# Performance work log

Hardware: AMD Instinct MI355X
Metric: run time of the kernel (lower is better)

## Reference

```python
import jax, jax.numpy as jnp
import numpy as np

D = 2048
H = 16
HD = D // H


def setup_inputs() -> dict:
    key = jax.random.key(0)
    k1, k2, k3 = jax.random.split(key, 3)
    x = jax.random.normal(k1, (2, 2048, D), dtype=jnp.float32)
    # torch Linear(d, 3d, bias=False): y = x @ W.T; store transposed weight [D, 3D]
    Wqkv = jax.random.normal(k2, (D, 3 * D), dtype=jnp.float32) * (D ** -0.5)
    Wo = jax.random.normal(k3, (D, D), dtype=jnp.float32) * (D ** -0.5)
    return {"x": x, "Wqkv": Wqkv, "Wo": Wo}


def reference(x, Wqkv, Wo):
    B, S, _ = x.shape
    qkv = (x @ Wqkv).reshape(B, S, 3, H, HD)
    q = qkv[:, :, 0].transpose(0, 2, 1, 3)  # [B,H,S,HD]
    k = qkv[:, :, 1].transpose(0, 2, 1, 3)
    v = qkv[:, :, 2].transpose(0, 2, 1, 3)
    scores = jnp.einsum("bhqd,bhkd->bhqk", q, k) * (HD ** -0.5)
    causal = jnp.tril(jnp.ones((S, S), dtype=bool))  # keep lower triangle
    scores = jnp.where(causal, scores, jnp.float32(-1e9))
    a = jax.nn.softmax(scores, axis=-1)
    o = jnp.einsum("bhqk,bhkd->bhqd", a, v)
    o = o.transpose(0, 2, 1, 3).reshape(B, S, H * HD)
    return o @ Wo
```

## Files before the change

kernel.cpp:

```cpp
#include <hip/hip_runtime.h>
#include <hip/hip_bf16.h>
#include <cstdint>

typedef __bf16 bf16;
typedef __bf16 bf16x8 __attribute__((ext_vector_type(8)));
typedef __bf16 bf16x4 __attribute__((ext_vector_type(4)));
typedef __bf16 bf16x2 __attribute__((ext_vector_type(2)));
typedef float floatx4 __attribute__((ext_vector_type(4)));
typedef float f32x16 __attribute__((ext_vector_type(16)));
typedef int intx4 __attribute__((ext_vector_type(4)));

#define MFMA16(a, b, c) __builtin_amdgcn_mfma_f32_16x16x32_bf16(a, b, c, 0, 0, 0)
#define MFMA32(a, b, c) __builtin_amdgcn_mfma_f32_32x32x16_bf16(a, b, c, 0, 0, 0)

__device__ __forceinline__ void gload_lds16(const void* g, void* l) {
    __builtin_amdgcn_global_load_lds(
        (const __attribute__((address_space(1))) void*)g,
        (__attribute__((address_space(3))) void*)l, 16, 0, 0);
}

__device__ __forceinline__ int pack2(float a, float b) {
    union { bf16x2 v; int u; } z;
    z.v[0] = (bf16)a;
    z.v[1] = (bf16)b;
    return z.u;
}

__global__ void downcast_kernel(const float* __restrict__ in, bf16* __restrict__ out,
                                size_t n) {
    const size_t i = ((size_t)blockIdx.x * blockDim.x + threadIdx.x) * 4;
    if (i >= n) return;
    const float4 v = *(const float4*)(in + i);
    bf16x4 o = {(bf16)v.x, (bf16)v.y, (bf16)v.z, (bf16)v.w};
    *(bf16x4*)(out + i) = o;
}

__global__ void transpose_kernel(const float* __restrict__ in, bf16* __restrict__ out,
                                 int R, int C) {
    __shared__ float tile[32][33];
    const int c0 = blockIdx.x * 32, r0 = blockIdx.y * 32;
    const int tx = threadIdx.x & 31, ty = threadIdx.x >> 5;
    for (int i = 0; i < 32; i += 8)
        tile[ty + i][tx] = in[(size_t)(r0 + ty + i) * C + (c0 + tx)];
    __syncthreads();
    for (int i = 0; i < 32; i += 8)
        out[(size_t)(c0 + ty + i) * R + (r0 + tx)] = (bf16)tile[tx][ty + i];
}

template <int MODE>
__global__ __launch_bounds__(256) void gemm_bt_kernel(
    const bf16* __restrict__ A, const bf16* __restrict__ BT,
    int M, int N, int K,
    bf16* __restrict__ qt, bf16* __restrict__ kt, bf16* __restrict__ vt,
    float* __restrict__ Cout) {
    __shared__ alignas(16) bf16 As[128 * 64];
    __shared__ alignas(16) bf16 Bs[128 * 64];

    const int tid = threadIdx.x;
    const int wave = tid >> 6, lane = tid & 63;
    const int quad = lane >> 4, r16 = lane & 15;
    const int m0 = blockIdx.y * 128, n0 = blockIdx.x * 128;
    const int wm = (wave >> 1) * 64, wn = (wave & 1) * 64;

    int srow[4], soff[4];
#pragma unroll
    for (int j = 0; j < 4; ++j) {
        const int c = tid + j * 256;
        srow[j] = c >> 3;
        soff[j] = ((c & 7) ^ (srow[j] & 7)) * 8;
    }

    floatx4 acc[4][4] = {};

    for (int k0 = 0; k0 < K; k0 += 64) {
        __syncthreads();
#pragma unroll
        for (int j = 0; j < 4; ++j) {
            const int c = tid + j * 256;
            gload_lds16(A + (size_t)(m0 + srow[j]) * K + k0 + soff[j], As + c * 8);
            gload_lds16(BT + (size_t)(n0 + srow[j]) * K + k0 + soff[j], Bs + c * 8);
        }
        __syncthreads();

#pragma unroll
        for (int kc = 0; kc < 2; ++kc) {
            bf16x8 a[4], b[4];
#pragma unroll
            for (int i = 0; i < 4; ++i) {
                const int row = wm + i * 16 + r16;
                const int sp = (4 * kc + quad) ^ (row & 7);
                a[i] = *(const bf16x8*)(As + row * 64 + sp * 8);
            }
#pragma unroll
            for (int j = 0; j < 4; ++j) {
                const int row = wn + j * 16 + r16;
                const int sp = (4 * kc + quad) ^ (row & 7);
                b[j] = *(const bf16x8*)(Bs + row * 64 + sp * 8);
            }
#pragma unroll
            for (int i = 0; i < 4; ++i)
#pragma unroll
                for (int j = 0; j < 4; ++j)
                    acc[i][j] = MFMA16(a[i], b[j], acc[i][j]);
        }
    }

    if (MODE == 0) {
        const int t = n0 >> 11;
        const float qscale = 0.08838834764831845f;
#pragma unroll
        for (int i = 0; i < 4; ++i) {
            const int mbase = m0 + wm + i * 16 + quad * 4;
            const int b_ = mbase >> 11;
            const int s = mbase & 2047;
#pragma unroll
            for (int j = 0; j < 4; ++j) {
                const int n = n0 + wn + j * 16 + r16;
                const int h = (n >> 7) & 15, hd = n & 127;
                const int bh = b_ * 16 + h;
                if (t == 0) {
#pragma unroll
                    for (int r = 0; r < 4; ++r)
                        qt[(size_t)(bh * 2048 + s + r) * 128 + hd] =
                            (bf16)(acc[i][j][r] * qscale);
                } else if (t == 1) {
#pragma unroll
                    for (int r = 0; r < 4; ++r)
                        kt[(size_t)(bh * 2048 + s + r) * 128 + hd] = (bf16)acc[i][j][r];
                } else {
                    bf16x4 pv = {(bf16)acc[i][j][0], (bf16)acc[i][j][1],
                                 (bf16)acc[i][j][2], (bf16)acc[i][j][3]};
                    *(bf16x4*)(vt + (size_t)(bh * 128 + hd) * 2048 + s) = pv;
                }
            }
        }
    } else {
#pragma unroll
        for (int i = 0; i < 4; ++i) {
            const int mbase = m0 + wm + i * 16 + quad * 4;
#pragma unroll
            for (int j = 0; j < 4; ++j) {
                const int n = n0 + wn + j * 16 + r16;
#pragma unroll
                for (int r = 0; r < 4; ++r)
                    Cout[(size_t)(mbase + r) * N + n] = acc[i][j][r];
            }
        }
    }
}

__global__ __launch_bounds__(256, 2) void attn_kernel(
    const bf16* __restrict__ qt, const bf16* __restrict__ kt,
    const bf16* __restrict__ vt, bf16* __restrict__ o) {
    __shared__ alignas(16) bf16 Ks[2][64 * 128];
    __shared__ alignas(16) bf16 Vts[2][128 * 64];

    const int tid = threadIdx.x;
    const int wave = tid >> 6, lane = tid & 63;
    const int l31 = lane & 31, h = lane >> 5;
    const int bh = blockIdx.x, by = blockIdx.y;
    const int t = by < 8 ? by : 23 - by;
    const int b_ = bh >> 4, hh = bh & 15;

    const int q0 = t * 128;
    const int qbase = q0 + wave * 32;
    const int qrow = qbase + l31;

    bf16x8 aq[8];
    {
        const bf16* qr = qt + (((size_t)bh * 2048 + qrow) << 7);
#pragma unroll
        for (int s = 0; s < 8; ++s)
            aq[s] = *(const bf16x8*)(qr + s * 16 + h * 8);
    }

    auto stageKV = [&](int buf, int k0) {
#pragma unroll
        for (int j = 0; j < 4; ++j) {
            const int c = tid + j * 256;
            const int row = c >> 4, sp = c & 15, s = sp ^ (row & 15);
            gload_lds16(kt + (((size_t)bh * 2048 + k0 + row) << 7) + s * 8,
                        &Ks[buf][c * 8]);
        }
#pragma unroll
        for (int j = 0; j < 4; ++j) {
            const int c = tid + j * 256;
            const int row = c >> 3, sp = c & 7, s = sp ^ (row & 7);
            gload_lds16(vt + ((size_t)bh * 128 + row) * 2048 + k0 + s * 8,
                        &Vts[buf][c * 8]);
        }
    };

    f32x16 oacc[4] = {};
    float lsum = 0.f;

    const int nit = 2 * t + 2;
    stageKV(0, 0);
    __syncthreads();
    int cur = 0;

    for (int it = 0; it < nit; ++it) {
        if (it + 1 < nit) stageKV(cur ^ 1, (it + 1) * 64);
        const int k0 = it * 64;

        if (k0 <= qbase + 31) {
            const bf16* Kc = &Ks[cur][0];
            const bf16* Vc = &Vts[cur][0];

            f32x16 sacc[2] = {};
            __builtin_amdgcn_s_setprio(1);
#pragma unroll
            for (int nt = 0; nt < 2; ++nt) {
#pragma unroll
                for (int s = 0; s < 8; ++s) {
                    const int sp = (2 * s + h) ^ (l31 & 15);
                    bf16x8 bk = *(const bf16x8*)(Kc + (nt * 32 + l31) * 128 + sp * 8);
                    sacc[nt] = MFMA32(bk, aq[s], sacc[nt]);
                }
            }
            __builtin_amdgcn_s_setprio(0);

            const bool needmask = (k0 + 63) > qbase;
            bf16x8 ap[4];
#pragma unroll
            for (int s4 = 0; s4 < 4; ++s4) {
                const int nt = s4 >> 1, base = (s4 & 1) * 8;
                float e[8];
#pragma unroll
                for (int k = 0; k < 8; ++k) {
                    const int c = base + k;
                    const int key = k0 + nt * 32 + (c & 3) + 8 * (c >> 2) + 4 * h;
                    float v = __expf(sacc[nt][c]);
                    if (needmask && key > qrow) v = 0.f;
                    e[k] = v;
                    lsum += v;
                }
                const int X0 = pack2(e[0], e[1]), X1 = pack2(e[2], e[3]);
                const int Y0 = pack2(e[4], e[5]), Y1 = pack2(e[6], e[7]);
                int W0 = h ? X0 : Y0, W1 = h ? X1 : Y1;
                W0 = __shfl_xor(W0, 32);
                W1 = __shfl_xor(W1, 32);
                union { intx4 w; bf16x8 v; } u;
                u.w[0] = h ? W0 : X0;
                u.w[1] = h ? W1 : X1;
                u.w[2] = h ? Y0 : W0;
                u.w[3] = h ? Y1 : W1;
                ap[s4] = u.v;
            }

            __builtin_amdgcn_s_setprio(1);
#pragma unroll
            for (int d0 = 0; d0 < 4; ++d0) {
#pragma unroll
                for (int ks = 0; ks < 4; ++ks) {
                    const int sp = (2 * ks + h) ^ (l31 & 7);
                    bf16x8 bv = *(const bf16x8*)(Vc + (d0 * 32 + l31) * 64 + sp * 8);
                    oacc[d0] = MFMA32(ap[ks], bv, oacc[d0]);
                }
            }
            __builtin_amdgcn_s_setprio(0);
        }

        __syncthreads();
        cur ^= 1;
    }

    lsum += __shfl_xor(lsum, 32);
    const float inv = 1.0f / lsum;
    float invr[16];
#pragma unroll
    for (int r = 0; r < 16; ++r)
        invr[r] = __shfl(inv, (r & 3) + 8 * (r >> 2) + 4 * h, 32);

#pragma unroll
    for (int d0 = 0; d0 < 4; ++d0) {
#pragma unroll
        for (int r = 0; r < 16; ++r) {
            const int rr = (r & 3) + 8 * (r >> 2) + 4 * h;
            o[(size_t)(b_ * 2048 + qbase + rr) * 2048 + hh * 128 + d0 * 32 + l31] =
                (bf16)(oacc[d0][r] * invr[r]);
        }
    }
}

extern "C" void kernel_launch(void* const* d_in, const int* in_sizes, int n_in,
                              void* d_out, int out_size, void* d_ws, size_t ws_size,
                              hipStream_t stream) {
    const float* x    = (const float*)d_in[0];
    const float* Wqkv = (const float*)d_in[1];
    const float* Wo   = (const float*)d_in[2];
    float* out        = (float*)d_out;

    char* ws = (char*)d_ws;
    bf16* xb    = (bf16*)ws; ws += (size_t)4096 * 2048 * 2;
    bf16* WqkvT = (bf16*)ws; ws += (size_t)6144 * 2048 * 2;
    bf16* WoT   = (bf16*)ws; ws += (size_t)2048 * 2048 * 2;
    bf16* qt    = (bf16*)ws; ws += (size_t)32 * 2048 * 128 * 2;
    bf16* kt    = (bf16*)ws; ws += (size_t)32 * 2048 * 128 * 2;
    bf16* vt    = (bf16*)ws; ws += (size_t)32 * 128 * 2048 * 2;
    bf16* ob    = (bf16*)ws; ws += (size_t)4096 * 2048 * 2;

    downcast_kernel<<<8192, 256, 0, stream>>>(x, xb, (size_t)4096 * 2048);
    transpose_kernel<<<dim3(192, 64), 256, 0, stream>>>(Wqkv, WqkvT, 2048, 6144);
    transpose_kernel<<<dim3(64, 64), 256, 0, stream>>>(Wo, WoT, 2048, 2048);

    gemm_bt_kernel<0><<<dim3(48, 32), 256, 0, stream>>>(
        xb, WqkvT, 4096, 6144, 2048, qt, kt, vt, nullptr);

    attn_kernel<<<dim3(32, 16), 256, 0, stream>>>(qt, kt, vt, ob);

    gemm_bt_kernel<1><<<dim3(16, 32), 256, 0, stream>>>(
        ob, WoT, 4096, 2048, 2048, nullptr, nullptr, nullptr, out);
}
```

Baseline: 375.2 us.

## Add 256x256 double-buffered QKV GEMM and fuse prep kernels into one launch

Replaces the 128x128 QKV projection GEMM with a 512-thread 256x256 tile kernel. It double-buffers LDS via direct global-to-LDS loads, uses XOR swizzling, raises priority around MFMA phases, and remaps blocks in a swizzled order for L2 locality. The downcast and two transpose kernels are merged into one launch to cut launch overhead. The larger tile raises arithmetic intensity, at the cost of 128KB LDS and one block per CU with only 384 blocks. The epilogue also applies the query scale at store time.

Measured after the change: 387.4 us. +3.3%, slower.

```diff
diff --git a/kernel.cpp b/kernel.cpp
--- a/kernel.cpp
+++ b/kernel.cpp
@@ -19,6 +19,11 @@
         (__attribute__((address_space(3))) void*)l, 16, 0, 0);
 }
 
+#define BARRIER()     asm volatile("s_barrier" ::: "memory")
+#define WAIT_LGKM0()  do { asm volatile("s_waitcnt lgkmcnt(0)" ::: "memory"); \
+                           __builtin_amdgcn_sched_barrier(0); } while (0)
+#define WAIT_VM(N)    asm volatile("s_waitcnt vmcnt(" #N ")" ::: "memory")
+
 __device__ __forceinline__ int pack2(float a, float b) {
     union { bf16x2 v; int u; } z;
     z.v[0] = (bf16)a;
@@ -26,25 +31,207 @@
     return z.u;
 }
 
-__global__ void downcast_kernel(const float* __restrict__ in, bf16* __restrict__ out,
-                                size_t n) {
-    const size_t i = ((size_t)blockIdx.x * blockDim.x + threadIdx.x) * 4;
-    if (i >= n) return;
-    const float4 v = *(const float4*)(in + i);
-    bf16x4 o = {(bf16)v.x, (bf16)v.y, (bf16)v.z, (bf16)v.w};
-    *(bf16x4*)(out + i) = o;
-}
-
-__global__ void transpose_kernel(const float* __restrict__ in, bf16* __restrict__ out,
-                                 int R, int C) {
+__global__ __launch_bounds__(256) void prep_kernel(
+    const float* __restrict__ x, const float* __restrict__ Wqkv,
+    const float* __restrict__ Wo, bf16* __restrict__ xb,
+    bf16* __restrict__ WqkvT, bf16* __restrict__ WoT) {
     __shared__ float tile[32][33];
-    const int c0 = blockIdx.x * 32, r0 = blockIdx.y * 32;
-    const int tx = threadIdx.x & 31, ty = threadIdx.x >> 5;
+    const int bid = blockIdx.x;
+    const int tid = threadIdx.x;
+
+    if (bid < 8192) {
+        const size_t i = ((size_t)bid * 256 + tid) * 4;
+        const float4 v = *(const float4*)(x + i);
+        bf16x4 o = {(bf16)v.x, (bf16)v.y, (bf16)v.z, (bf16)v.w};
+        *(bf16x4*)(xb + i) = o;
+        return;
+    }
+
+    const float* in;
+    bf16* out;
+    int R, C, bx, by;
+    if (bid < 20480) {
+        const int b = bid - 8192;
+        in = Wqkv; out = WqkvT; R = 2048; C = 6144;
+        bx = b % 192; by = b / 192;
+    } else {
+        const int b = bid - 20480;
+        in = Wo; out = WoT; R = 2048; C = 2048;
+        bx = b & 63; by = b >> 6;
+    }
+    const int c0 = bx * 32, r0 = by * 32;
+    const int tx = tid & 31, ty = tid >> 5;
     for (int i = 0; i < 32; i += 8)
         tile[ty + i][tx] = in[(size_t)(r0 + ty + i) * C + (c0 + tx)];
     __syncthreads();
     for (int i = 0; i < 32; i += 8)
         out[(size_t)(c0 + ty + i) * R + (r0 + tx)] = (bf16)tile[tx][ty + i];
+}
+
+__global__ __launch_bounds__(512, 1) void gemm256_qkv_kernel(
+    const bf16* __restrict__ A, const bf16* __restrict__ BT, int K,
+    bf16* __restrict__ qt, bf16* __restrict__ kt, bf16* __restrict__ vt) {
+    __shared__ alignas(16) bf16 As[2][16384];
+    __shared__ alignas(16) bf16 Bs[2][16384];
+
+    const int tid = threadIdx.x;
+    const int wave = tid >> 6, lane = tid & 63;
+    const int quad = lane >> 4, r16 = lane & 15;
+
+    const int flat = blockIdx.y * 24 + blockIdx.x;
+    const int swz = (flat & 7) * 48 + (flat >> 3);
+    const int n0 = (swz % 24) << 8, m0 = (swz / 24) << 8;
+
+    const int wm = (wave >> 2) << 7;
+    const int wn = (wave & 3) << 6;
+
+    auto stageTile = [&](int buf, int kt_) {
+#pragma unroll
+        for (int hf = 0; hf < 2; ++hf)
+#pragma unroll
+            for (int j = 0; j < 2; ++j) {
+                const int c = tid + j * 512;
+                const int row = c >> 3;
+                const int soff = ((c & 7) ^ (row & 7)) * 8;
+                gload_lds16(A + (size_t)(m0 + hf * 128 + row) * K + kt_ * 64 + soff,
+                            &As[buf][hf * 8192 + c * 8]);
+            }
+#pragma unroll
+        for (int hf = 0; hf < 2; ++hf)
+#pragma unroll
+            for (int j = 0; j < 2; ++j) {
+                const int c = tid + j * 512;
+                const int row = c >> 3;
+                const int soff = ((c & 7) ^ (row & 7)) * 8;
+                gload_lds16(BT + (size_t)(n0 + hf * 128 + row) * K + kt_ * 64 + soff,
+                            &Bs[buf][hf * 8192 + c * 8]);
+            }
+    };
+
+    floatx4 acc[8][4] = {};
+    const int NT = K >> 6;
+
+    stageTile(0, 0);
+    stageTile(1, 1);
+    WAIT_VM(8);
+    BARRIER();
+
+    for (int t = 0; t < NT; ++t) {
+        const int bsel = t & 1;
+        const bf16* Ab = &As[bsel][0];
+        const bf16* Bb = &Bs[bsel][0];
+        bf16x8 alo[4][2], ahi[4][2], blo[2][2], bhi[2][2];
+
+#pragma unroll
+        for (int i = 0; i < 4; ++i) {
+            const int row = wm + i * 16 + r16;
+#pragma unroll
+            for (int kc = 0; kc < 2; ++kc)
+                alo[i][kc] = *(const bf16x8*)(Ab + row * 64 + (((4 * kc + quad) ^ (row & 7)) << 3));
+        }
+#pragma unroll
+        for (int j = 0; j < 2; ++j) {
+            const int row = wn + j * 16 + r16;
+#pragma unroll
+            for (int kc = 0; kc < 2; ++kc)
+                blo[j][kc] = *(const bf16x8*)(Bb + row * 64 + (((4 * kc + quad) ^ (row & 7)) << 3));
+        }
+        BARRIER();
+        WAIT_LGKM0();
+        __builtin_amdgcn_s_setprio(1);
+#pragma unroll
+        for (int i = 0; i < 4; ++i)
+#pragma unroll
+            for (int j = 0; j < 2; ++j)
+#pragma unroll
+                for (int kc = 0; kc < 2; ++kc)
+                    acc[i][j] = MFMA16(alo[i][kc], blo[j][kc], acc[i][j]);
+        __builtin_amdgcn_s_setprio(0);
+        BARRIER();
+
+#pragma unroll
+        for (int j = 0; j < 2; ++j) {
+            const int row = wn + (2 + j) * 16 + r16;
+#pragma unroll
+            for (int kc = 0; kc < 2; ++kc)
+                bhi[j][kc] = *(const bf16x8*)(Bb + row * 64 + (((4 * kc + quad) ^ (row & 7)) << 3));
+        }
+        BARRIER();
+        WAIT_LGKM0();
+        __builtin_amdgcn_s_setprio(1);
+#pragma unroll
+        for (int i = 0; i < 4; ++i)
+#pragma unroll
+            for (int j = 0; j < 2; ++j)
+#pragma unroll
+                for (int kc = 0; kc < 2; ++kc)
+                    acc[i][2 + j] = MFMA16(alo[i][kc], bhi[j][kc], acc[i][2 + j]);
+        __builtin_amdgcn_s_setprio(0);
+        BARRIER();
+
+#pragma unroll
+        for (int i = 0; i < 4; ++i) {
+            const int row = wm + (4 + i) * 16 + r16;
+#pragma unroll
+            for (int kc = 0; kc < 2; ++kc)
+                ahi[i][kc] = *(const bf16x8*)(Ab + row * 64 + (((4 * kc + quad) ^ (row & 7)) << 3));
+        }
+        BARRIER();
+        WAIT_LGKM0();
+        __builtin_amdgcn_s_setprio(1);
+#pragma unroll
+        for (int i = 0; i < 4; ++i)
+#pragma unroll
+            for (int j = 0; j < 2; ++j)
+#pragma unroll
+                for (int kc = 0; kc < 2; ++kc)
+                    acc[4 + i][2 + j] = MFMA16(ahi[i][kc], bhi[j][kc], acc[4 + i][2 + j]);
+        __builtin_amdgcn_s_setprio(0);
+        BARRIER();
+
+        if (t + 2 < NT) stageTile(bsel, t + 2);
+        __builtin_amdgcn_s_setprio(1);
+#pragma unroll
+        for (int i = 0; i < 4; ++i)
+#pragma unroll
+            for (int j = 0; j < 2; ++j)
+#pragma unroll
+                for (int kc = 0; kc < 2; ++kc)
+                    acc[4 + i][j] = MFMA16(ahi[i][kc], blo[j][kc], acc[4 + i][j]);
+        __builtin_amdgcn_s_setprio(0);
+        if (t + 2 < NT) WAIT_VM(8);
+        else           WAIT_VM(0);
+        BARRIER();
+    }
+
+    const int tsel = n0 >> 11;
+    const float qscale = 0.08838834764831845f;
+#pragma unroll
+    for (int i = 0; i < 8; ++i) {
+        const int mbase = m0 + wm + i * 16 + quad * 4;
+        const int b_ = mbase >> 11;
+        const int s = mbase & 2047;
+#pragma unroll
+        for (int j = 0; j < 4; ++j) {
+            const int n = n0 + wn + j * 16 + r16;
+            const int h = (n >> 7) & 15, hd = n & 127;
+            const int bh = b_ * 16 + h;
+            if (tsel == 0) {
+#pragma unroll
+                for (int r = 0; r < 4; ++r)
+                    qt[(size_t)(bh * 2048 + s + r) * 128 + hd] =
+                        (bf16)(acc[i][j][r] * qscale);
+            } else if (tsel == 1) {
+#pragma unroll
+                for (int r = 0; r < 4; ++r)
+                    kt[(size_t)(bh * 2048 + s + r) * 128 + hd] = (bf16)acc[i][j][r];
+            } else {
+                bf16x4 pv = {(bf16)acc[i][j][0], (bf16)acc[i][j][1],
+                             (bf16)acc[i][j][2], (bf16)acc[i][j][3]};
+                *(bf16x4*)(vt + (size_t)(bh * 128 + hd) * 2048 + s) = pv;
+            }
+        }
+    }
 }
 
 template <int MODE>
@@ -300,12 +487,10 @@
     bf16* vt    = (bf16*)ws; ws += (size_t)32 * 128 * 2048 * 2;
     bf16* ob    = (bf16*)ws; ws += (size_t)4096 * 2048 * 2;
 
-    downcast_kernel<<<8192, 256, 0, stream>>>(x, xb, (size_t)4096 * 2048);
-    transpose_kernel<<<dim3(192, 64), 256, 0, stream>>>(Wqkv, WqkvT, 2048, 6144);
-    transpose_kernel<<<dim3(64, 64), 256, 0, stream>>>(Wo, WoT, 2048, 2048);
-
-    gemm_bt_kernel<0><<<dim3(48, 32), 256, 0, stream>>>(
-        xb, WqkvT, 4096, 6144, 2048, qt, kt, vt, nullptr);
+    prep_kernel<<<24576, 256, 0, stream>>>(x, Wqkv, Wo, xb, WqkvT, WoT);
+
+    gemm256_qkv_kernel<<<dim3(24, 16), 512, 0, stream>>>(
+        xb, WqkvT, 2048, qt, kt, vt);
 
     attn_kernel<<<dim3(32, 16), 256, 0, stream>>>(qt, kt, vt, ob);
 
```
